# Optimization experiments

Hardware: AMD Instinct MI355X
Metric: run time of the kernel (lower is better)

Reference implementation:

```python
import jax, jax.numpy as jnp
import numpy as np

N_LVL = 127  # 8-bit symmetric: levels in [-128, 127]
BN_EPS = 1e-5


def ste_round(x):
    # straight-through estimator round (HAWQ uses STE for quantization)
    return x + jax.lax.stop_gradient(jnp.round(x) - x)


def quant_act(x):
    # symmetric per-tensor 8-bit activation quantization (QuantAct)
    s = jax.lax.stop_gradient(jnp.max(jnp.abs(x))) / N_LVL
    xq = jnp.clip(ste_round(x / s), -N_LVL - 1, N_LVL) * s
    return xq, s


def q_incept_conv(x, a_sf, w, g, b, m, v, stride, pad):
    # QuantBnConv2d: fold BN into conv, per-out-channel symmetric int8 weights
    std = jnp.sqrt(v + BN_EPS)
    wf = w * (g / std)[:, None, None, None]          # folded weight [O,I,kh,kw]
    bf = b - g * m / std                              # folded bias  [O]
    w_sf = jax.lax.stop_gradient(jnp.max(jnp.abs(wf), axis=(1, 2, 3))) / N_LVL
    wq = jnp.clip(ste_round(wf / w_sf[:, None, None, None]), -N_LVL - 1, N_LVL) * w_sf[:, None, None, None]
    conv_sf = a_sf * w_sf                             # per-channel output scale
    bq = ste_round(bf / conv_sf) * conv_sf            # bias quantized to conv scale
    y = jax.lax.conv_general_dilated(
        x, wq, window_strides=(stride, stride), padding=pad,
        dimension_numbers=('NCHW', 'OIHW', 'NCHW'))
    y = jax.nn.relu(y + bq[None, :, None, None])
    return quant_act(y)  # requantize activation (QuantAct with pre-scale)


def setup_inputs() -> dict:
    key = jax.random.key(0)
    ks = jax.random.split(key, 32)
    d = {}
    d['x'] = jax.random.normal(ks[0], (64, 384, 17, 17), jnp.float32)
    shapes = {
        'w1': (448, 384, 1, 1), 'w2': (384, 448, 3, 3),
        'w3': (384, 384, 1, 3), 'w4': (384, 384, 3, 1),
    }
    chans = {'1': 448, '2': 384, '3': 384, '4': 384}
    i = 1
    for idx in ['1', '2', '3', '4']:
        c = chans[idx]
        d['w' + idx] = jax.random.normal(ks[i], shapes['w' + idx], jnp.float32) * 0.05; i += 1
        d['g' + idx] = jax.random.uniform(ks[i], (c,), jnp.float32, 0.5, 1.5); i += 1
        d['b' + idx] = jax.random.normal(ks[i], (c,), jnp.float32) * 0.1; i += 1
        d['m' + idx] = jax.random.normal(ks[i], (c,), jnp.float32) * 0.1; i += 1
        d['v' + idx] = jax.random.uniform(ks[i], (c,), jnp.float32, 0.5, 1.5); i += 1
    return d


def reference(x, w1, g1, b1, m1, v1, w2, g2, b2, m2, v2,
              w3, g3, b3, m3, v3, w4, g4, b4, m4, v4):
    # q_input_act
    x, a_sf = quant_act(x)
    # conv_list: conv1 (1x1, 384->448), conv2 (3x3, 448->384, pad 1)
    x, a_sf = q_incept_conv(x, a_sf, w1, g1, b1, m1, v1, 1, [(0, 0), (0, 0)])
    x, a_sf = q_incept_conv(x, a_sf, w2, g2, b2, m2, v2, 1, [(1, 1), (1, 1)])
    # parallel branches
    y1, s1 = q_incept_conv(x, a_sf, w3, g3, b3, m3, v3, 1, [(0, 0), (1, 1)])  # 1x3
    y2, s2 = q_incept_conv(x, a_sf, w4, g4, b4, m4, v4, 1, [(1, 1), (0, 0)])  # 3x1
    # concat + rescaling requant (q_rescaling_activ): both branches already
    # dequantized floats; requantize to a single common scale
    cat = jnp.concatenate([y1, y2], axis=1)  # [N, 768, H, W]
    out, _ = quant_act(cat)
    return out
```

## Files before the change

kernel.cpp:

```cpp
#include <hip/hip_runtime.h>
#include <stdint.h>

#define NLVL 127.0f
#define NPOS (64 * 289)

typedef int v4i __attribute__((ext_vector_type(4)));
typedef int v16i __attribute__((ext_vector_type(16)));
typedef unsigned int uint;

__device__ __forceinline__ int swz_wg(int bid, int nwg) {
    const int q = nwg >> 3, r = nwg & 7;
    const int xcd = bid & 7;
    const int base = xcd < r ? xcd * (q + 1) : r * (q + 1) + (xcd - r) * q;
    return base + (bid >> 3);
}

__global__ __launch_bounds__(256) void amax_abs_kernel(const float* __restrict__ x,
                                                       int n, float* __restrict__ slot) {
    __shared__ float red[256];
    float lm = 0.f;
    for (int i = blockIdx.x * 256 + threadIdx.x; i < n; i += gridDim.x * 256)
        lm = fmaxf(lm, fabsf(x[i]));
    red[threadIdx.x] = lm;
    __syncthreads();
    for (int s = 128; s > 0; s >>= 1) {
        if (threadIdx.x < s) red[threadIdx.x] = fmaxf(red[threadIdx.x], red[threadIdx.x + s]);
        __syncthreads();
    }
    if (threadIdx.x == 0) atomicMax((unsigned int*)slot, __float_as_uint(red[0]));
}

__global__ __launch_bounds__(256) void quant_x_kernel(const float* __restrict__ x,
                                                      signed char* __restrict__ n0,
                                                      const float* __restrict__ scal) {
    __shared__ uint t32[64][97];
    const float s = scal[0] / NLVL;
    const int tid = threadIdx.x;
    const int pi = tid & 63;
    const int pos = blockIdx.x * 64 + pi;
    const int n = pos / 289;
    const int hw = pos - n * 289;
    const float* xb = x + (size_t)n * 384 * 289 + hw;
    for (int cq = tid >> 6; cq < 96; cq += 4) {
        uint pk = 0;
#pragma unroll
        for (int k = 0; k < 4; ++k) {
            const float f = xb[(size_t)(cq * 4 + k) * 289];
            float q = rintf(f / s);
            q = fminf(fmaxf(q, -128.f), 127.f);
            pk |= ((uint)((int)q & 0xff)) << (8 * k);
        }
        t32[pi][cq] = pk;
    }
    __syncthreads();
    for (int k = 0; k < 6; ++k) {
        const int c16 = (tid >> 6) + k * 4;
        uint4 v;
        v.x = t32[pi][c16 * 4 + 0];
        v.y = t32[pi][c16 * 4 + 1];
        v.z = t32[pi][c16 * 4 + 2];
        v.w = t32[pi][c16 * 4 + 3];
        *(uint4*)&n0[((size_t)c16 * NPOS + pos) * 16] = v;
    }
}

__global__ __launch_bounds__(256) void wq_kernel(
    const float* __restrict__ w1, const float* __restrict__ g1, const float* __restrict__ b1,
    const float* __restrict__ m1, const float* __restrict__ v1, signed char* __restrict__ s1w,
    float* __restrict__ s1sf, float* __restrict__ s1bf,
    const float* __restrict__ w2, const float* __restrict__ g2, const float* __restrict__ b2,
    const float* __restrict__ m2, const float* __restrict__ v2, signed char* __restrict__ s2w,
    float* __restrict__ s2sf, float* __restrict__ s2bf,
    const float* __restrict__ w3, const float* __restrict__ g3, const float* __restrict__ b3,
    const float* __restrict__ m3, const float* __restrict__ v3, signed char* __restrict__ s3w,
    float* __restrict__ s3sf, float* __restrict__ s3bf,
    const float* __restrict__ w4, const float* __restrict__ g4, const float* __restrict__ b4,
    const float* __restrict__ m4, const float* __restrict__ v4, signed char* __restrict__ s4w,
    float* __restrict__ s4sf, float* __restrict__ s4bf) {
    const int bid = blockIdx.x;
    const float *w, *g, *b, *m, *v;
    signed char* wstg;
    float *wsf, *bfv;
    int I, KHW, OCP, GPT, o;
    if (bid < 448) {
        w = w1; g = g1; b = b1; m = m1; v = v1; wstg = s1w; wsf = s1sf; bfv = s1bf;
        I = 384; KHW = 1; OCP = 512; GPT = 24; o = bid;
    } else if (bid < 832) {
        w = w2; g = g2; b = b2; m = m2; v = v2; wstg = s2w; wsf = s2sf; bfv = s2bf;
        I = 448; KHW = 9; OCP = 384; GPT = 28; o = bid - 448;
    } else if (bid < 1216) {
        w = w3; g = g3; b = b3; m = m3; v = v3; wstg = s3w; wsf = s3sf; bfv = s3bf;
        I = 384; KHW = 3; OCP = 384; GPT = 24; o = bid - 832;
    } else {
        w = w4; g = g4; b = b4; m = m4; v = v4; wstg = s4w; wsf = s4sf; bfv = s4bf;
        I = 384; KHW = 3; OCP = 384; GPT = 24; o = bid - 1216;
    }
    const int E = I * KHW;
    __shared__ float red[256];
    const float std_ = sqrtf(v[o] + 1e-5f);
    const float fac = g[o] / std_;
    float lm = 0.f;
    for (int e = threadIdx.x; e < E; e += 256)
        lm = fmaxf(lm, fabsf(w[(size_t)o * E + e] * fac));
    red[threadIdx.x] = lm;
    __syncthreads();
    for (int s = 128; s > 0; s >>= 1) {
        if (threadIdx.x < s) red[threadIdx.x] = fmaxf(red[threadIdx.x], red[threadIdx.x + s]);
        __syncthreads();
    }
    const float w_sf = red[0] / NLVL;
    for (int e = threadIdx.x; e < E; e += 256) {
        const float wf = w[(size_t)o * E + e] * fac;
        float q = rintf(wf / w_sf);
        q = fminf(fmaxf(q, -128.f), 127.f);
        const int i = e / KHW;
        const int r = e - i * KHW;
        wstg[((size_t)(r * GPT + (i >> 4)) * OCP + o) * 16 + (i & 15)] = (signed char)q;
    }
    if (threadIdx.x == 0) {
        wsf[o] = w_sf;
        bfv[o] = b[o] - g[o] * m[o] / std_;
    }
}

template <int CINP, int COUT, int OCP, int KH, int KW, int PH, int PW>
__global__ __launch_bounds__(256) void qconv_mfma(
    const signed char* __restrict__ xin, const signed char* __restrict__ wstg,
    const float* __restrict__ wsf, const float* __restrict__ bfv,
    const float* __restrict__ scal, int sidx,
    float* __restrict__ yout, float* __restrict__ amax_slot,
    const signed char* __restrict__ zero16, int coff16) {
    constexpr int KCN = CINP / 64;
    constexpr int GPT = CINP / 16;
    constexpr int NKT = KH * KW * KCN;
    constexpr int NOC = OCP / 128;
    constexpr int NPB = 145;
    __shared__ float red[256];

    const int tid = threadIdx.x;
    const int lane = tid & 63;
    const int wid = tid >> 6;
    const int l31 = lane & 31;
    const int lh = lane >> 5;

    const int wgid = swz_wg(blockIdx.x, NPB * NOC);
    const int pb = wgid / NOC;
    const int ob = wgid - pb * NOC;
    const int p_blk = pb * 128;
    const int oc_blk = ob * 128;

    int pn[2], ph_[2], pw_[2];
    bool prowok[2];
#pragma unroll
    for (int it = 0; it < 2; ++it) {
        const int myp = p_blk + (wid >> 1) * 64 + it * 32 + l31;
        prowok[it] = myp < NPOS;
        const int pc = prowok[it] ? myp : 0;
        pn[it] = pc / 289;
        const int hw = pc - pn[it] * 289;
        ph_[it] = hw / 17;
        pw_[it] = hw - ph_[it] * 17;
    }
    const int oc_col0 = oc_blk + (wid & 1) * 64 + l31;

    auto loadA = [&](int kt, v4i (&a)[2][2]) {
        const int tap = kt / KCN;
        const int kc = kt - tap * KCN;
        const int kh = tap / KW;
        const int kw = tap - kh * KW;
#pragma unroll
        for (int it = 0; it < 2; ++it) {
            const int ih = ph_[it] + kh - PH;
            const int iw = pw_[it] + kw - PW;
            const bool ok = prowok[it] & ((unsigned)ih < 17u) & ((unsigned)iw < 17u);
            const int spos = pn[it] * 289 + ih * 17 + iw;
#pragma unroll
            for (int ks = 0; ks < 2; ++ks) {
                const signed char* p =
                    ok ? xin + ((size_t)((kc * 4 + ks * 2 + lh) * NPOS + spos)) * 16 : zero16;
                a[ks][it] = *(const v4i*)p;
            }
        }
    };
    auto loadB = [&](int kt, v4i (&b)[2][2]) {
        const int tap = kt / KCN;
        const int kc = kt - tap * KCN;
        const signed char* base =
            wstg + ((size_t)(tap * GPT + kc * 4 + lh) * OCP + oc_col0) * 16;
        b[0][0] = *(const v4i*)(base);
        b[0][1] = *(const v4i*)(base + 32 * 16);
        b[1][0] = *(const v4i*)(base + (size_t)2 * OCP * 16);
        b[1][1] = *(const v4i*)(base + (size_t)2 * OCP * 16 + 32 * 16);
    };

    v16i accE[2][2] = {}, accO[2][2] = {};

    auto compute = [&](const v4i (&a)[2][2], const v4i (&b)[2][2]) {
        accE[0][0] = __builtin_amdgcn_mfma_i32_32x32x32_i8(a[0][0], b[0][0], accE[0][0], 0, 0, 0);
        accE[0][1] = __builtin_amdgcn_mfma_i32_32x32x32_i8(a[0][0], b[0][1], accE[0][1], 0, 0, 0);
        accE[1][0] = __builtin_amdgcn_mfma_i32_32x32x32_i8(a[0][1], b[0][0], accE[1][0], 0, 0, 0);
        accE[1][1] = __builtin_amdgcn_mfma_i32_32x32x32_i8(a[0][1], b[0][1], accE[1][1], 0, 0, 0);
        accO[0][0] = __builtin_amdgcn_mfma_i32_32x32x32_i8(a[1][0], b[1][0], accO[0][0], 0, 0, 0);
        accO[0][1] = __builtin_amdgcn_mfma_i32_32x32x32_i8(a[1][0], b[1][1], accO[0][1], 0, 0, 0);
        accO[1][0] = __builtin_amdgcn_mfma_i32_32x32x32_i8(a[1][1], b[1][0], accO[1][0], 0, 0, 0);
        accO[1][1] = __builtin_amdgcn_mfma_i32_32x32x32_i8(a[1][1], b[1][1], accO[1][1], 0, 0, 0);
    };

    v4i aA[2][2], bA[2][2], aB[2][2], bB[2][2];
    loadA(0, aA);
    loadB(0, bA);
    for (int kt = 0; kt < NKT; kt += 2) {
        if (kt + 1 < NKT) {
            loadA(kt + 1, aB);
            loadB(kt + 1, bB);
        }
        compute(aA, bA);
        if (kt + 1 < NKT) {
            if (kt + 2 < NKT) {
                loadA(kt + 2, aA);
                loadB(kt + 2, bA);
            }
            compute(aB, bB);
        }
    }

    const float a_sf = scal[sidx] / NLVL;
    float csf[2];
    int bb[2], ocv[2];
#pragma unroll
    for (int jt = 0; jt < 2; ++jt) {
        const int oc = oc_blk + (wid & 1) * 64 + jt * 32 + l31;
        ocv[jt] = oc;
        const bool real = oc < COUT;
        const float wsfv = real ? wsf[oc] : 0.f;
        csf[jt] = a_sf * wsfv;
        bb[jt] = real ? (int)rintf(bfv[oc] / csf[jt]) : 0;
    }
    float lm = 0.f;
#pragma unroll
    for (int it = 0; it < 2; ++it) {
#pragma unroll
        for (int reg = 0; reg < 16; ++reg) {
            const int prow_o =
                p_blk + (wid >> 1) * 64 + it * 32 + (reg & 3) + 8 * (reg >> 2) + 4 * lh;
            const bool pok = prow_o < NPOS;
#pragma unroll
            for (int jt = 0; jt < 2; ++jt) {
                int t2 = accE[it][jt][reg] + accO[it][jt][reg] + bb[jt];
                t2 = t2 > 0 ? t2 : 0;
                const float v2 = csf[jt] * (float)t2;
                if (pok && ocv[jt] < COUT) {
                    lm = fmaxf(lm, v2);
                    yout[((size_t)(coff16 + (ocv[jt] >> 4)) * NPOS + prow_o) * 16 +
                         (ocv[jt] & 15)] = v2;
                }
            }
        }
    }
    red[tid] = lm;
    __syncthreads();
    for (int s = 128; s > 0; s >>= 1) {
        if (tid < s) red[tid] = fmaxf(red[tid], red[tid + s]);
        __syncthreads();
    }
    if (tid == 0) atomicMax((unsigned int*)amax_slot, __float_as_uint(red[0]));
}

__global__ __launch_bounds__(256) void qconv_dual(
    const signed char* __restrict__ xin, const signed char* __restrict__ wstg3,
    const signed char* __restrict__ wstg4,
    const float* __restrict__ wsf3, const float* __restrict__ bf3,
    const float* __restrict__ wsf4, const float* __restrict__ bf4,
    const float* __restrict__ scal, int sidx,
    float* __restrict__ yout, float* __restrict__ amax_slot,
    const signed char* __restrict__ zero16) {
    constexpr int KCN = 6;
    constexpr int GPT = 24;
    constexpr int OCP = 384;
    constexpr int NKT = 3 * KCN;
    constexpr int NOC = 3;
    constexpr int NPB = 145;
    __shared__ float red[256];

    const int tid = threadIdx.x;
    const int lane = tid & 63;
    const int wid = tid >> 6;
    const int l31 = lane & 31;
    const int lh = lane >> 5;

    const int wgid = swz_wg(blockIdx.x, NPB * NOC);
    const int pb = wgid / NOC;
    const int ob = wgid - pb * NOC;
    const int p_blk = pb * 128;
    const int oc_blk = ob * 128;

    int pn[2], ph_[2], pw_[2];
    bool prowok[2];
#pragma unroll
    for (int it = 0; it < 2; ++it) {
        const int myp = p_blk + (wid >> 1) * 64 + it * 32 + l31;
        prowok[it] = myp < NPOS;
        const int pc = prowok[it] ? myp : 0;
        pn[it] = pc / 289;
        const int hw = pc - pn[it] * 289;
        ph_[it] = hw / 17;
        pw_[it] = hw - ph_[it] * 17;
    }
    const int oc_col0 = oc_blk + (wid & 1) * 64 + l31;

    auto loadA = [&](int dh, int dw, int kc, v4i (&a)[2][2]) {
#pragma unroll
        for (int it = 0; it < 2; ++it) {
            const int ih = ph_[it] + dh;
            const int iw = pw_[it] + dw;
            const bool ok = prowok[it] & ((unsigned)ih < 17u) & ((unsigned)iw < 17u);
            const int spos = pn[it] * 289 + ih * 17 + iw;
#pragma unroll
            for (int ks = 0; ks < 2; ++ks) {
                const signed char* p =
                    ok ? xin + ((size_t)((kc * 4 + ks * 2 + lh) * NPOS + spos)) * 16 : zero16;
                a[ks][it] = *(const v4i*)p;
            }
        }
    };
    auto loadB = [&](const signed char* wstg, int tap, int kc, v4i (&b)[2][2]) {
        const signed char* base =
            wstg + ((size_t)(tap * GPT + kc * 4 + lh) * OCP + oc_col0) * 16;
        b[0][0] = *(const v4i*)(base);
        b[0][1] = *(const v4i*)(base + 32 * 16);
        b[1][0] = *(const v4i*)(base + (size_t)2 * OCP * 16);
        b[1][1] = *(const v4i*)(base + (size_t)2 * OCP * 16 + 32 * 16);
    };

    v16i acc3[2][2] = {}, acc4[2][2] = {};

    auto compute = [&](v16i (&acc)[2][2], const v4i (&a)[2][2], const v4i (&b)[2][2]) {
#pragma unroll
        for (int ks = 0; ks < 2; ++ks) {
            acc[0][0] = __builtin_amdgcn_mfma_i32_32x32x32_i8(a[ks][0], b[ks][0], acc[0][0], 0, 0, 0);
            acc[0][1] = __builtin_amdgcn_mfma_i32_32x32x32_i8(a[ks][0], b[ks][1], acc[0][1], 0, 0, 0);
            acc[1][0] = __builtin_amdgcn_mfma_i32_32x32x32_i8(a[ks][1], b[ks][0], acc[1][0], 0, 0, 0);
            acc[1][1] = __builtin_amdgcn_mfma_i32_32x32x32_i8(a[ks][1], b[ks][1], acc[1][1], 0, 0, 0);
        }
    };

    for (int kt = 0; kt < NKT; ++kt) {
        const int tap = kt / KCN;
        const int kc = kt - tap * KCN;
        v4i a3[2][2], a4[2][2], b3[2][2], b4[2][2];
        loadA(0, tap - 1, kc, a3);
        loadA(tap - 1, 0, kc, a4);
        loadB(wstg3, tap, kc, b3);
        loadB(wstg4, tap, kc, b4);
        compute(acc3, a3, b3);
        compute(acc4, a4, b4);
    }

    const float a_sf = scal[sidx] / NLVL;
    float csf3[2], csf4[2];
    int bb3[2], bb4[2], ocv[2];
#pragma unroll
    for (int jt = 0; jt < 2; ++jt) {
        const int oc = oc_blk + (wid & 1) * 64 + jt * 32 + l31;
        ocv[jt] = oc;
        csf3[jt] = a_sf * wsf3[oc];
        bb3[jt] = (int)rintf(bf3[oc] / csf3[jt]);
        csf4[jt] = a_sf * wsf4[oc];
        bb4[jt] = (int)rintf(bf4[oc] / csf4[jt]);
    }
    float lm = 0.f;
#pragma unroll
    for (int it = 0; it < 2; ++it) {
#pragma unroll
        for (int reg = 0; reg < 16; ++reg) {
            const int prow_o =
                p_blk + (wid >> 1) * 64 + it * 32 + (reg & 3) + 8 * (reg >> 2) + 4 * lh;
            const bool pok = prow_o < NPOS;
#pragma unroll
            for (int jt = 0; jt < 2; ++jt) {
                int t3 = acc3[it][jt][reg] + bb3[jt];
                t3 = t3 > 0 ? t3 : 0;
                const float v3v = csf3[jt] * (float)t3;
                int t4 = acc4[it][jt][reg] + bb4[jt];
                t4 = t4 > 0 ? t4 : 0;
                const float v4v = csf4[jt] * (float)t4;
                if (pok) {
                    lm = fmaxf(lm, fmaxf(v3v, v4v));
                    const size_t sl = (size_t)(ocv[jt] >> 4);
                    yout[(sl * NPOS + prow_o) * 16 + (ocv[jt] & 15)] = v3v;
                    yout[(((size_t)24 + sl) * NPOS + prow_o) * 16 + (ocv[jt] & 15)] = v4v;
                }
            }
        }
    }
    red[tid] = lm;
    __syncthreads();
    for (int s = 128; s > 0; s >>= 1) {
        if (tid < s) red[tid] = fmaxf(red[tid], red[tid + s]);
        __syncthreads();
    }
    if (tid == 0) atomicMax((unsigned int*)amax_slot, __float_as_uint(red[0]));
}

__global__ __launch_bounds__(256) void requant_kernel(const float* __restrict__ f,
                                                      signed char* __restrict__ q,
                                                      const float* __restrict__ scal,
                                                      int idx, int nvec) {
    const float s = scal[idx] / NLVL;
    for (int i = blockIdx.x * 256 + threadIdx.x; i < nvec; i += gridDim.x * 256) {
        const float4 v = ((const float4*)f)[i];
        const int b0 = (int)fminf(fmaxf(rintf(v.x / s), -128.f), 127.f);
        const int b1 = (int)fminf(fmaxf(rintf(v.y / s), -128.f), 127.f);
        const int b2 = (int)fminf(fmaxf(rintf(v.z / s), -128.f), 127.f);
        const int b3 = (int)fminf(fmaxf(rintf(v.w / s), -128.f), 127.f);
        ((unsigned int*)q)[i] =
            (b0 & 0xff) | ((b1 & 0xff) << 8) | ((b2 & 0xff) << 16) | ((b3 & 0xff) << 24);
    }
}

__global__ __launch_bounds__(256) void transpose_requant_kernel(
    const float* __restrict__ f, float* __restrict__ out,
    const float* __restrict__ scal, int idx) {
    __shared__ float tile[64][65];
    const float s = scal[idx] / NLVL;
    const int tid = threadIdx.x;
    const int w = tid >> 6, l = tid & 63;
    const int pt = blockIdx.x % 289, ct = blockIdx.x / 289;
    const int pos0 = pt * 64, c0 = ct * 64;
    const int slab = ct * 4 + w;
#pragma unroll
    for (int j = 0; j < 4; ++j) {
        const int p = (l >> 2) + j * 16;
        const int co = (l & 3) * 4;
        const float4 v = *(const float4*)&f[((size_t)slab * NPOS + pos0 + p) * 16 + co];
        tile[p][w * 16 + co + 0] = v.x;
        tile[p][w * 16 + co + 1] = v.y;
        tile[p][w * 16 + co + 2] = v.z;
        tile[p][w * 16 + co + 3] = v.w;
    }
    __syncthreads();
    const int pos = pos0 + l;
    const int n = pos / 289;
    const int hw = pos - n * 289;
#pragma unroll
    for (int k = 0; k < 16; ++k) {
        const int c = c0 + w * 16 + k;
        float v = tile[l][w * 16 + k];
        v = fminf(fmaxf(rintf(v / s), -128.f), 127.f) * s;
        out[((size_t)(n * 768 + c)) * 289 + hw] = v;
    }
}

extern "C" void kernel_launch(void* const* d_in, const int* in_sizes, int n_in,
                              void* d_out, int out_size, void* d_ws, size_t ws_size,
                              hipStream_t stream) {
    const float* x  = (const float*)d_in[0];
    const float* w1 = (const float*)d_in[1];
    const float* g1 = (const float*)d_in[2];
    const float* b1 = (const float*)d_in[3];
    const float* m1 = (const float*)d_in[4];
    const float* v1 = (const float*)d_in[5];
    const float* w2 = (const float*)d_in[6];
    const float* g2 = (const float*)d_in[7];
    const float* b2 = (const float*)d_in[8];
    const float* m2 = (const float*)d_in[9];
    const float* v2 = (const float*)d_in[10];
    const float* w3 = (const float*)d_in[11];
    const float* g3 = (const float*)d_in[12];
    const float* b3 = (const float*)d_in[13];
    const float* m3 = (const float*)d_in[14];
    const float* v3 = (const float*)d_in[15];
    const float* w4 = (const float*)d_in[16];
    const float* g4 = (const float*)d_in[17];
    const float* b4 = (const float*)d_in[18];
    const float* m4 = (const float*)d_in[19];
    const float* v4 = (const float*)d_in[20];
    float* out = (float*)d_out;
    char* ws = (char*)d_ws;

    size_t off = 0;
    auto take = [&](size_t bytes) {
        char* p = ws + off;
        off = (off + bytes + 255) & ~(size_t)255;
        return p;
    };
    float* scal = (float*)take(64);
    const signed char* zero16 = (const signed char*)(scal + 8);
    signed char* wstg1 = (signed char*)take((size_t)24 * 512 * 16);
    float* sf1 = (float*)take(448 * 4);
    float* bf1 = (float*)take(448 * 4);
    signed char* wstg2 = (signed char*)take((size_t)9 * 28 * 384 * 16);
    float* sf2 = (float*)take(384 * 4);
    float* bf2 = (float*)take(384 * 4);
    signed char* wstg3 = (signed char*)take((size_t)3 * 24 * 384 * 16);
    float* sf3 = (float*)take(384 * 4);
    float* bf3 = (float*)take(384 * 4);
    signed char* wstg4 = (signed char*)take((size_t)3 * 24 * 384 * 16);
    float* sf4 = (float*)take(384 * 4);
    float* bf4 = (float*)take(384 * 4);
    signed char* n0 = (signed char*)take((size_t)24 * NPOS * 16);
    signed char* q1 = (signed char*)take((size_t)28 * NPOS * 16);
    signed char* q2 = (signed char*)take((size_t)24 * NPOS * 16);
    float* fbuf = (float*)take((size_t)48 * NPOS * 16 * 4);

    hipMemsetAsync(scal, 0, 64, stream);
    hipMemsetAsync(wstg1, 0, (size_t)24 * 512 * 16, stream);

    wq_kernel<<<1600, 256, 0, stream>>>(w1, g1, b1, m1, v1, wstg1, sf1, bf1,
                                        w2, g2, b2, m2, v2, wstg2, sf2, bf2,
                                        w3, g3, b3, m3, v3, wstg3, sf3, bf3,
                                        w4, g4, b4, m4, v4, wstg4, sf4, bf4);

    amax_abs_kernel<<<1024, 256, 0, stream>>>(x, 64 * 384 * 289, scal + 0);
    quant_x_kernel<<<289, 256, 0, stream>>>(x, n0, scal);

    qconv_mfma<384, 448, 512, 1, 1, 0, 0>
        <<<145 * 4, 256, 0, stream>>>(n0, wstg1, sf1, bf1, scal, 0, fbuf, scal + 1, zero16, 0);
    requant_kernel<<<2048, 256, 0, stream>>>(fbuf, q1, scal, 1, 28 * NPOS * 16 / 4);

    qconv_mfma<448, 384, 384, 3, 3, 1, 1>
        <<<145 * 3, 256, 0, stream>>>(q1, wstg2, sf2, bf2, scal, 1, fbuf, scal + 2, zero16, 0);
    requant_kernel<<<2048, 256, 0, stream>>>(fbuf, q2, scal, 2, 24 * NPOS * 16 / 4);

    qconv_dual<<<145 * 3, 256, 0, stream>>>(q2, wstg3, wstg4, sf3, bf3, sf4, bf4,
                                            scal, 2, fbuf, scal + 3, zero16);

    transpose_requant_kernel<<<289 * 12, 256, 0, stream>>>(fbuf, out, scal, 3);
}
```

Before: 254.9 us.

## Use triple-buffered register prefetch and split dual-branch conv into per-branch workgroups

The generic int8 MFMA conv loop now prefetches three K-steps ahead in rotating register buffers with a single accumulator set, replacing the two-stage ping-pong with even/odd accumulators. The fused 1x3/3x1 branch kernel is split so each workgroup handles one branch, which doubles the grid and halves per-workgroup accumulator and load state. This is meant to hide global load latency better and raise occupancy and parallelism, at the cost of more register buffers for prefetch and twice as many blocks. Each branch workgroup now reads its input tile separately, so shared input reuse between the two branches is lost.

```diff
diff --git a/kernel.cpp b/kernel.cpp
--- a/kernel.cpp
+++ b/kernel.cpp
@@ -133,6 +133,7 @@
     constexpr int KCN = CINP / 64;
     constexpr int GPT = CINP / 16;
     constexpr int NKT = KH * KW * KCN;
+    static_assert(NKT % 3 == 0, "depth-3 rotation needs NKT % 3 == 0");
     constexpr int NOC = OCP / 128;
     constexpr int NPB = 145;
     __shared__ float red[256];
@@ -193,35 +194,29 @@
         b[1][1] = *(const v4i*)(base + (size_t)2 * OCP * 16 + 32 * 16);
     };
 
-    v16i accE[2][2] = {}, accO[2][2] = {};
+    v16i acc[2][2] = {};
 
     auto compute = [&](const v4i (&a)[2][2], const v4i (&b)[2][2]) {
-        accE[0][0] = __builtin_amdgcn_mfma_i32_32x32x32_i8(a[0][0], b[0][0], accE[0][0], 0, 0, 0);
-        accE[0][1] = __builtin_amdgcn_mfma_i32_32x32x32_i8(a[0][0], b[0][1], accE[0][1], 0, 0, 0);
-        accE[1][0] = __builtin_amdgcn_mfma_i32_32x32x32_i8(a[0][1], b[0][0], accE[1][0], 0, 0, 0);
-        accE[1][1] = __builtin_amdgcn_mfma_i32_32x32x32_i8(a[0][1], b[0][1], accE[1][1], 0, 0, 0);
-        accO[0][0] = __builtin_amdgcn_mfma_i32_32x32x32_i8(a[1][0], b[1][0], accO[0][0], 0, 0, 0);
-        accO[0][1] = __builtin_amdgcn_mfma_i32_32x32x32_i8(a[1][0], b[1][1], accO[0][1], 0, 0, 0);
-        accO[1][0] = __builtin_amdgcn_mfma_i32_32x32x32_i8(a[1][1], b[1][0], accO[1][0], 0, 0, 0);
-        accO[1][1] = __builtin_amdgcn_mfma_i32_32x32x32_i8(a[1][1], b[1][1], accO[1][1], 0, 0, 0);
-    };
-
-    v4i aA[2][2], bA[2][2], aB[2][2], bB[2][2];
-    loadA(0, aA);
-    loadB(0, bA);
-    for (int kt = 0; kt < NKT; kt += 2) {
-        if (kt + 1 < NKT) {
-            loadA(kt + 1, aB);
-            loadB(kt + 1, bB);
-        }
+#pragma unroll
+        for (int ks = 0; ks < 2; ++ks) {
+            acc[0][0] = __builtin_amdgcn_mfma_i32_32x32x32_i8(a[ks][0], b[ks][0], acc[0][0], 0, 0, 0);
+            acc[0][1] = __builtin_amdgcn_mfma_i32_32x32x32_i8(a[ks][0], b[ks][1], acc[0][1], 0, 0, 0);
+            acc[1][0] = __builtin_amdgcn_mfma_i32_32x32x32_i8(a[ks][1], b[ks][0], acc[1][0], 0, 0, 0);
+            acc[1][1] = __builtin_amdgcn_mfma_i32_32x32x32_i8(a[ks][1], b[ks][1], acc[1][1], 0, 0, 0);
+        }
+    };
+
+    v4i aA[2][2], bA[2][2], aB[2][2], bB[2][2], aC[2][2], bC[2][2];
+    loadA(0, aA); loadB(0, bA);
+    loadA(1, aB); loadB(1, bB);
+    loadA(2, aC); loadB(2, bC);
+    for (int kt = 0; kt < NKT; kt += 3) {
         compute(aA, bA);
-        if (kt + 1 < NKT) {
-            if (kt + 2 < NKT) {
-                loadA(kt + 2, aA);
-                loadB(kt + 2, bA);
-            }
-            compute(aB, bB);
-        }
+        if (kt + 3 < NKT) { loadA(kt + 3, aA); loadB(kt + 3, bA); }
+        compute(aB, bB);
+        if (kt + 4 < NKT) { loadA(kt + 4, aB); loadB(kt + 4, bB); }
+        compute(aC, bC);
+        if (kt + 5 < NKT) { loadA(kt + 5, aC); loadB(kt + 5, bC); }
     }
 
     const float a_sf = scal[sidx] / NLVL;
@@ -246,7 +241,7 @@
             const bool pok = prow_o < NPOS;
 #pragma unroll
             for (int jt = 0; jt < 2; ++jt) {
-                int t2 = accE[it][jt][reg] + accO[it][jt][reg] + bb[jt];
+                int t2 = acc[it][jt][reg] + bb[jt];
                 t2 = t2 > 0 ? t2 : 0;
                 const float v2 = csf[jt] * (float)t2;
                 if (pok && ocv[jt] < COUT) {
@@ -266,9 +261,9 @@
     if (tid == 0) atomicMax((unsigned int*)amax_slot, __float_as_uint(red[0]));
 }
 
-__global__ __launch_bounds__(256) void qconv_dual(
-    const signed char* __restrict__ xin, const signed char* __restrict__ wstg3,
-    const signed char* __restrict__ wstg4,
+__global__ __launch_bounds__(256) void qconv_br34(
+    const signed char* __restrict__ xin,
+    const signed char* __restrict__ wstg3, const signed char* __restrict__ wstg4,
     const float* __restrict__ wsf3, const float* __restrict__ bf3,
     const float* __restrict__ wsf4, const float* __restrict__ bf4,
     const float* __restrict__ scal, int sidx,
@@ -277,7 +272,8 @@
     constexpr int KCN = 6;
     constexpr int GPT = 24;
     constexpr int OCP = 384;
-    constexpr int NKT = 3 * KCN;
+    constexpr int COUT = 384;
+    constexpr int NKT = 18;
     constexpr int NOC = 3;
     constexpr int NPB = 145;
     __shared__ float red[256];
@@ -288,11 +284,18 @@
     const int l31 = lane & 31;
     const int lh = lane >> 5;
 
-    const int wgid = swz_wg(blockIdx.x, NPB * NOC);
-    const int pb = wgid / NOC;
-    const int ob = wgid - pb * NOC;
+    const int wk = swz_wg(blockIdx.x, NPB * NOC * 2);
+    const int br = wk & 1;
+    const int pair = wk >> 1;
+    const int pb = pair / NOC;
+    const int ob = pair - pb * NOC;
     const int p_blk = pb * 128;
     const int oc_blk = ob * 128;
+
+    const signed char* wstg = br ? wstg4 : wstg3;
+    const float* wsf = br ? wsf4 : wsf3;
+    const float* bfv = br ? bf4 : bf3;
+    const int coff16 = br ? 24 : 0;
 
     int pn[2], ph_[2], pw_[2];
     bool prowok[2];
@@ -308,7 +311,11 @@
     }
     const int oc_col0 = oc_blk + (wid & 1) * 64 + l31;
 
-    auto loadA = [&](int dh, int dw, int kc, v4i (&a)[2][2]) {
+    auto loadA = [&](int kt, v4i (&a)[2][2]) {
+        const int tap = kt / KCN;
+        const int kc = kt - tap * KCN;
+        const int dh = br ? (tap - 1) : 0;
+        const int dw = br ? 0 : (tap - 1);
 #pragma unroll
         for (int it = 0; it < 2; ++it) {
             const int ih = ph_[it] + dh;
@@ -323,7 +330,9 @@
             }
         }
     };
-    auto loadB = [&](const signed char* wstg, int tap, int kc, v4i (&b)[2][2]) {
+    auto loadB = [&](int kt, v4i (&b)[2][2]) {
+        const int tap = kt / KCN;
+        const int kc = kt - tap * KCN;
         const signed char* base =
             wstg + ((size_t)(tap * GPT + kc * 4 + lh) * OCP + oc_col0) * 16;
         b[0][0] = *(const v4i*)(base);
@@ -332,9 +341,9 @@
         b[1][1] = *(const v4i*)(base + (size_t)2 * OCP * 16 + 32 * 16);
     };
 
-    v16i acc3[2][2] = {}, acc4[2][2] = {};
-
-    auto compute = [&](v16i (&acc)[2][2], const v4i (&a)[2][2], const v4i (&b)[2][2]) {
+    v16i acc[2][2] = {};
+
+    auto compute = [&](const v4i (&a)[2][2], const v4i (&b)[2][2]) {
 #pragma unroll
         for (int ks = 0; ks < 2; ++ks) {
             acc[0][0] = __builtin_amdgcn_mfma_i32_32x32x32_i8(a[ks][0], b[ks][0], acc[0][0], 0, 0, 0);
@@ -344,29 +353,28 @@
         }
     };
 
-    for (int kt = 0; kt < NKT; ++kt) {
-        const int tap = kt / KCN;
-        const int kc = kt - tap * KCN;
-        v4i a3[2][2], a4[2][2], b3[2][2], b4[2][2];
-        loadA(0, tap - 1, kc, a3);
-        loadA(tap - 1, 0, kc, a4);
-        loadB(wstg3, tap, kc, b3);
-        loadB(wstg4, tap, kc, b4);
-        compute(acc3, a3, b3);
-        compute(acc4, a4, b4);
+    v4i aA[2][2], bA[2][2], aB[2][2], bB[2][2], aC[2][2], bC[2][2];
+    loadA(0, aA); loadB(0, bA);
+    loadA(1, aB); loadB(1, bB);
+    loadA(2, aC); loadB(2, bC);
+    for (int kt = 0; kt < NKT; kt += 3) {
+        compute(aA, bA);
+        if (kt + 3 < NKT) { loadA(kt + 3, aA); loadB(kt + 3, bA); }
+        compute(aB, bB);
+        if (kt + 4 < NKT) { loadA(kt + 4, aB); loadB(kt + 4, bB); }
+        compute(aC, bC);
+        if (kt + 5 < NKT) { loadA(kt + 5, aC); loadB(kt + 5, bC); }
     }
 
     const float a_sf = scal[sidx] / NLVL;
-    float csf3[2], csf4[2];
-    int bb3[2], bb4[2], ocv[2];
+    float csf[2];
+    int bb[2], ocv[2];
 #pragma unroll
     for (int jt = 0; jt < 2; ++jt) {
         const int oc = oc_blk + (wid & 1) * 64 + jt * 32 + l31;
         ocv[jt] = oc;
-        csf3[jt] = a_sf * wsf3[oc];
-        bb3[jt] = (int)rintf(bf3[oc] / csf3[jt]);
-        csf4[jt] = a_sf * wsf4[oc];
-        bb4[jt] = (int)rintf(bf4[oc] / csf4[jt]);
+        csf[jt] = a_sf * wsf[oc];
+        bb[jt] = (int)rintf(bfv[oc] / csf[jt]);
     }
     float lm = 0.f;
 #pragma unroll
@@ -378,17 +386,13 @@
             const bool pok = prow_o < NPOS;
 #pragma unroll
             for (int jt = 0; jt < 2; ++jt) {
-                int t3 = acc3[it][jt][reg] + bb3[jt];
-                t3 = t3 > 0 ? t3 : 0;
-                const float v3v = csf3[jt] * (float)t3;
-                int t4 = acc4[it][jt][reg] + bb4[jt];
-                t4 = t4 > 0 ? t4 : 0;
-                const float v4v = csf4[jt] * (float)t4;
+                int t2 = acc[it][jt][reg] + bb[jt];
+                t2 = t2 > 0 ? t2 : 0;
+                const float v2 = csf[jt] * (float)t2;
                 if (pok) {
-                    lm = fmaxf(lm, fmaxf(v3v, v4v));
-                    const size_t sl = (size_t)(ocv[jt] >> 4);
-                    yout[(sl * NPOS + prow_o) * 16 + (ocv[jt] & 15)] = v3v;
-                    yout[(((size_t)24 + sl) * NPOS + prow_o) * 16 + (ocv[jt] & 15)] = v4v;
+                    lm = fmaxf(lm, v2);
+                    yout[((size_t)(coff16 + (ocv[jt] >> 4)) * NPOS + prow_o) * 16 +
+                         (ocv[jt] & 15)] = v2;
                 }
             }
         }
@@ -522,8 +526,8 @@
         <<<145 * 3, 256, 0, stream>>>(q1, wstg2, sf2, bf2, scal, 1, fbuf, scal + 2, zero16, 0);
     requant_kernel<<<2048, 256, 0, stream>>>(fbuf, q2, scal, 2, 24 * NPOS * 16 / 4);
 
-    qconv_dual<<<145 * 3, 256, 0, stream>>>(q2, wstg3, wstg4, sf3, bf3, sf4, bf4,
-                                            scal, 2, fbuf, scal + 3, zero16);
+    qconv_br34<<<145 * 3 * 2, 256, 0, stream>>>(q2, wstg3, wstg4, sf3, bf3, sf4, bf4,
+                                                scal, 2, fbuf, scal + 3, zero16);
 
     transpose_requant_kernel<<<289 * 12, 256, 0, stream>>>(fbuf, out, scal, 3);
 }
```

Measured after the change: 225.8 us. 11.4% less time.
